# Optimization experiments

Hardware: AMD Instinct MI355X
Metric: run time of the kernel (lower is better)

## Reference

```python
import jax, jax.numpy as jnp
from jax import lax
import numpy as np

BN_EPS = 1e-5

def _bn(x, g, b, m, v):
    # inference-mode BatchNorm1d (running stats)
    return (x - m) * (g / jnp.sqrt(v + BN_EPS)) + b

def _mlp2(x, W1, g, b, m, v, W2):
    # Linear(no bias) -> BN -> ReLU -> (Dropout off in eval) -> Linear(no bias)
    h = jax.nn.relu(_bn(x @ W1.T, g, b, m, v))
    return h @ W2.T

def setup_inputs() -> dict:
    key = jax.random.key(0)
    ks = iter(jax.random.split(key, 40))
    B, N = 1024, 10
    f32 = jnp.float32
    def w(shape, s=0.02):
        return jax.random.normal(next(ks), shape, f32) * s
    def bn_params(c):
        return (jnp.ones((c,), f32), jnp.zeros((c,), f32),
                jax.random.normal(next(ks), (c,), f32) * 0.1,
                jax.random.uniform(next(ks), (c,), f32, 0.5, 1.5))
    inp = {
        'features_object': jax.random.normal(next(ks), (B, N, 1024), f32),
        'bbox': jax.random.uniform(next(ks), (B, N, 4), f32),
        'word_embedding': jax.random.normal(next(ks), (B, N, 300), f32),
        'sentiment': jax.random.normal(next(ks), (B, N, 4096), f32),
        'body': jax.random.normal(next(ks), (B, 2048), f32),
    }
    # mlp_object: 1024 -> 128 -> 128
    inp['W1_o'] = w((128, 1024)); inp['g_o'], inp['b_o'], inp['m_o'], inp['v_o'] = bn_params(128)
    inp['W2_o'] = w((128, 128))
    # mlp_sentiment: 4096 -> 512 -> 128
    inp['W1_s'] = w((512, 4096)); inp['g_s'], inp['b_s'], inp['m_s'], inp['v_s'] = bn_params(512)
    inp['W2_s'] = w((128, 512))
    # mlp_body: 2048 -> 256 -> 128
    inp['W1_b'] = w((256, 2048)); inp['g_b'], inp['b_b'], inp['m_b'], inp['v_b'] = bn_params(256)
    inp['W2_b'] = w((128, 256))
    # channel attention (CBAM-style, in_planes=10, ratio=2): shared MLP 10->5->10
    inp['Wc1'] = w((5, 10), 0.3)
    inp['Wc2'] = w((10, 5), 0.3)
    # spatial attention: Conv1d(2 -> 1, k=7, pad=3, no bias)
    inp['Wsa'] = w((1, 2, 7), 0.3)
    # fc1: 688 -> 256 (with bias) then BN
    inp['Wf'] = w((256, 688)); inp['bf'] = jnp.zeros((256,), f32)
    inp['g_f'], inp['b_f'], inp['m_f'], inp['v_f'] = bn_params(256)
    return inp

def reference(features_object, bbox, word_embedding, sentiment, body,
              W1_o, g_o, b_o, m_o, v_o, W2_o,
              W1_s, g_s, b_s, m_s, v_s, W2_s,
              W1_b, g_b, b_b, m_b, v_b, W2_b,
              Wc1, Wc2, Wsa, Wf, bf, g_f, b_f, m_f, v_f):
    B, N, _ = features_object.shape
    # per-slice MLPs batched into single GEMMs over B*N rows
    obj = _mlp2(features_object.reshape(B * N, -1), W1_o, g_o, b_o, m_o, v_o, W2_o).reshape(B, N, 128)
    sen = _mlp2(sentiment.reshape(B * N, -1), W1_s, g_s, b_s, m_s, v_s, W2_s).reshape(B, N, 128)
    # body is identical across the N repeats (inference BN), compute once and broadcast
    bod = _mlp2(body.reshape(B, -1), W1_b, g_b, b_b, m_b, v_b, W2_b)
    bod = jnp.broadcast_to(bod[:, None, :], (B, N, 128))
    x = jnp.concatenate([obj, bbox, word_embedding, sen, bod], axis=2)  # [B,N,688]
    # channel attention over the N-slice axis
    def ca_mlp(a):  # [B,N] -> [B,N]
        return jax.nn.relu(a @ Wc1.T) @ Wc2.T
    att_c = jax.nn.sigmoid(ca_mlp(x.mean(axis=2)) + ca_mlp(x.max(axis=2)))  # [B,N]
    x = x * att_c[:, :, None]
    # spatial attention along feature axis
    s = jnp.stack([x.mean(axis=1), x.max(axis=1)], axis=1)  # [B,2,688]
    sa = lax.conv_general_dilated(s, Wsa, (1,), [(3, 3)],
                                  dimension_numbers=('NCH', 'OIH', 'NCH'))  # [B,1,688]
    x = x * jax.nn.sigmoid(sa)
    x = x.sum(axis=1)  # [B,688]
    out = jax.nn.relu(_bn(x @ Wf.T + bf, g_f, b_f, m_f, v_f))  # [B,256]
    return out
```

## Files before the change

### kernel.cpp

```cpp
#include <hip/hip_runtime.h>
#include <hip/hip_bf16.h>
#include <math.h>

typedef __attribute__((ext_vector_type(8))) short short8;
typedef __attribute__((ext_vector_type(4))) float floatx4;

static __device__ __forceinline__ unsigned short f2bf(float f) {
    unsigned int u = __float_as_uint(f);
    unsigned int r = (u + 0x7fffu + ((u >> 16) & 1u)) >> 16;
    return (unsigned short)r;
}

static __device__ __forceinline__ void g2l16(const void* g, void* l) {
    __builtin_amdgcn_global_load_lds(
        (const __attribute__((address_space(1))) unsigned int*)g,
        (__attribute__((address_space(3))) unsigned int*)l,
        16, 0, 0);
}

struct GDesc {
    const float*          Af;
    const unsigned short* Ab;
    const unsigned short* W;
    float*          Cf;
    unsigned short* Cb;
    const float *bias, *g, *b, *m, *v;
    int M, N, K;
    int Kreal;
    int fuse;
    int nbx;
    int block0;
    int nbb;
    int ksplit;
};
struct GArgs { GDesc g[3]; int n; };

__global__ __launch_bounds__(256)
void gemm_grouped(GArgs ga)
{
    __shared__ unsigned short As[2][4096];
    __shared__ unsigned short Bs[2][4096];

    const int bid = blockIdx.x;
    int gi = 0;
    #pragma unroll
    for (int i = 1; i < 3; ++i)
        if (i < ga.n && bid >= ga.g[i].block0) gi = i;
    const GDesc d = ga.g[gi];

    int local = bid - d.block0;
    int kc = 0;
    int Kc = d.K;
    if (d.ksplit > 1) {
        Kc = d.K / d.ksplit;
        kc = local / d.nbb;
        local -= kc * d.nbb;
    }
    const int kbeg = kc * Kc;
    const int bx = local % d.nbx;
    const int by = local / d.nbx;
    const int row0 = by * 128;
    const int col0 = bx * 128;

    const int tid  = threadIdx.x;
    const int wave = tid >> 6;
    const int lane = tid & 63;
    const int qd   = lane >> 4;
    const int ln   = lane & 15;
    const int wr   = (wave >> 1) * 64;
    const int wc   = (wave & 1) * 64;

    const int c0 = wave * 128 + lane;
    const int c1 = c0 + 64;
    const int r0 = c0 >> 2, k0 = (c0 & 3) * 8;
    const int r1 = c1 >> 2, k1 = (c1 & 3) * 8;

    const int sr = tid >> 3;
    const int sc = (tid & 7) * 4;

    const bool afp = (d.Af != nullptr);
    const int niter = Kc >> 5;

    floatx4 acc[4][4];
    #pragma unroll
    for (int i = 0; i < 4; ++i)
        #pragma unroll
        for (int j = 0; j < 4; ++j) acc[i][j] = (floatx4){0.f, 0.f, 0.f, 0.f};

    g2l16(d.W + (size_t)(col0 + r0) * d.K + kbeg + k0, &Bs[0][(size_t)wave * 1024]);
    g2l16(d.W + (size_t)(col0 + r1) * d.K + kbeg + k1, &Bs[0][(size_t)wave * 1024 + 512]);
    float4 areg[4];
    if (afp) {
        #pragma unroll
        for (int p = 0; p < 4; ++p) {
            float4 v = (kbeg + sc < d.Kreal)
                ? *(const float4*)(d.Af + (size_t)(row0 + p * 32 + sr) * d.Kreal + kbeg + sc)
                : (float4){0.f, 0.f, 0.f, 0.f};
            ushort4 o = { f2bf(v.x), f2bf(v.y), f2bf(v.z), f2bf(v.w) };
            *(ushort4*)&As[0][(p * 32 + sr) * 32 + sc] = o;
        }
        if (niter > 1) {
            const int kg = kbeg + 32;
            #pragma unroll
            for (int p = 0; p < 4; ++p)
                areg[p] = (kg + sc < d.Kreal)
                    ? *(const float4*)(d.Af + (size_t)(row0 + p * 32 + sr) * d.Kreal + kg + sc)
                    : (float4){0.f, 0.f, 0.f, 0.f};
        }
    } else {
        g2l16(d.Ab + (size_t)(row0 + r0) * d.K + kbeg + k0, &As[0][(size_t)wave * 1024]);
        g2l16(d.Ab + (size_t)(row0 + r1) * d.K + kbeg + k1, &As[0][(size_t)wave * 1024 + 512]);
    }
    __syncthreads();

    int cur = 0;
    for (int it = 0; it < niter; ++it) {
        const int nxt = cur ^ 1;
        const bool pf = (it + 1 < niter);

        if (pf) {
            const int kg = kbeg + (it + 1) * 32;
            g2l16(d.W + (size_t)(col0 + r0) * d.K + kg + k0, &Bs[nxt][(size_t)wave * 1024]);
            g2l16(d.W + (size_t)(col0 + r1) * d.K + kg + k1, &Bs[nxt][(size_t)wave * 1024 + 512]);
            if (afp) {
                #pragma unroll
                for (int p = 0; p < 4; ++p) {
                    ushort4 o = { f2bf(areg[p].x), f2bf(areg[p].y),
                                  f2bf(areg[p].z), f2bf(areg[p].w) };
                    *(ushort4*)&As[nxt][(p * 32 + sr) * 32 + sc] = o;
                }
                if (it + 2 < niter) {
                    const int kg2 = kbeg + (it + 2) * 32;
                    #pragma unroll
                    for (int p = 0; p < 4; ++p)
                        areg[p] = (kg2 + sc < d.Kreal)
                            ? *(const float4*)(d.Af + (size_t)(row0 + p * 32 + sr) * d.Kreal + kg2 + sc)
                            : (float4){0.f, 0.f, 0.f, 0.f};
                }
            } else {
                g2l16(d.Ab + (size_t)(row0 + r0) * d.K + kg + k0, &As[nxt][(size_t)wave * 1024]);
                g2l16(d.Ab + (size_t)(row0 + r1) * d.K + kg + k1, &As[nxt][(size_t)wave * 1024 + 512]);
            }
        }

        short8 a[4], b[4];
        #pragma unroll
        for (int i = 0; i < 4; ++i)
            a[i] = *(const short8*)&As[cur][(wr + i * 16 + ln) * 32 + qd * 8];
        #pragma unroll
        for (int j = 0; j < 4; ++j)
            b[j] = *(const short8*)&Bs[cur][(wc + j * 16 + ln) * 32 + qd * 8];
        #pragma unroll
        for (int i = 0; i < 4; ++i)
            #pragma unroll
            for (int j = 0; j < 4; ++j)
                acc[i][j] = __builtin_amdgcn_mfma_f32_16x16x32_bf16(
                                a[i], b[j], acc[i][j], 0, 0, 0);

        __syncthreads();
        cur = nxt;
    }

    if (d.ksplit > 1) {
        #pragma unroll
        for (int j = 0; j < 4; ++j) {
            const int col = col0 + wc + j * 16 + ln;
            #pragma unroll
            for (int i = 0; i < 4; ++i) {
                #pragma unroll
                for (int r = 0; r < 4; ++r) {
                    const int row = row0 + wr + i * 16 + qd * 4 + r;
                    atomicAdd(&d.Cf[(size_t)row * d.N + col], acc[i][j][r]);
                }
            }
        }
        return;
    }

    #pragma unroll
    for (int j = 0; j < 4; ++j) {
        const int col = col0 + wc + j * 16 + ln;
        float add = d.bias ? d.bias[col] : 0.f;
        float scale = 1.f, shift = 0.f;
        if (d.fuse) {
            scale = d.g[col] * rsqrtf(d.v[col] + 1e-5f);
            shift = d.b[col] - d.m[col] * scale;
        }
        #pragma unroll
        for (int i = 0; i < 4; ++i) {
            #pragma unroll
            for (int r = 0; r < 4; ++r) {
                const int row = row0 + wr + i * 16 + qd * 4 + r;
                float vv = acc[i][j][r] + add;
                if (d.fuse) vv = fmaxf(vv * scale + shift, 0.f);
                if (d.Cf) d.Cf[(size_t)row * d.N + col] = vv;
                if (d.Cb) d.Cb[(size_t)row * d.N + col] = f2bf(vv);
            }
        }
    }
}

struct WSeg { const float* src; unsigned short* dst; int Kreal; int Kp; };
struct WArgs { WSeg s[7]; int off[8]; };

__global__ __launch_bounds__(256)
void cvt_weights(WArgs wa)
{
    int i = blockIdx.x * 256 + threadIdx.x;
    if (i >= wa.off[7]) return;
    int s = 0;
    #pragma unroll
    for (int j = 1; j < 7; ++j) if (i >= wa.off[j]) s = j;
    const WSeg sg = wa.s[s];
    const int li = i - wa.off[s];
    const int r = li / sg.Kp, c = li - r * sg.Kp;
    sg.dst[li] = (c < sg.Kreal) ? f2bf(sg.src[(size_t)r * sg.Kreal + c])
                                : (unsigned short)0;
}

struct FSeg { const float* src; unsigned short* dstb; float* dstf;
              const float *bias, *g, *b, *m, *v; int N; };
struct FArgs { FSeg s[3]; int off[4]; };

__global__ __launch_bounds__(256)
void bn_finalize(FArgs fa)
{
    int i = blockIdx.x * 256 + threadIdx.x;
    if (i >= fa.off[3]) return;
    int s = 0;
    #pragma unroll
    for (int j = 1; j < 3; ++j) if (i >= fa.off[j]) s = j;
    const FSeg sg = fa.s[s];
    const int li = i - fa.off[s];
    const int e = li * 4;
    const int col = e % sg.N;
    float4 vv = *(const float4*)(sg.src + e);
    float4 fo;
    ushort4 o;
    #pragma unroll
    for (int r = 0; r < 4; ++r) {
        float x = (&vv.x)[r];
        if (sg.bias) x += sg.bias[col + r];
        float sc = sg.g[col + r] * rsqrtf(sg.v[col + r] + 1e-5f);
        float sh = sg.b[col + r] - sg.m[col + r] * sc;
        x = fmaxf(x * sc + sh, 0.f);
        (&fo.x)[r] = x;
        ((unsigned short*)&o)[r] = f2bf(x);
    }
    if (sg.dstb) *(ushort4*)(sg.dstb + e) = o;
    if (sg.dstf) *(float4*)(sg.dstf + e) = fo;
}

__global__ __launch_bounds__(256)
void attn_kernel(const float* __restrict__ obj, const float* __restrict__ bbox,
                 const float* __restrict__ word, const float* __restrict__ sen,
                 const float* __restrict__ bod,
                 const float* __restrict__ Wc1, const float* __restrict__ Wc2,
                 const float* __restrict__ Wsa,
                 float* __restrict__ xsum_out)
{
    const int b = blockIdx.x;
    const int tid = threadIdx.x;

    __shared__ float xs[10][688];
    __shared__ float s0[688], s1[688];
    __shared__ float avec[10], mvec[10], att[10];
    __shared__ float cw[14], c1[50], c2[50];

    if (tid < 14) cw[tid] = Wsa[tid];
    if (tid < 50) { c1[tid] = Wc1[tid]; c2[tid] = Wc2[tid]; }

    for (int n = 0; n < 10; ++n) {
        const float* o  = obj  + ((size_t)b * 10 + n) * 128;
        const float* bx = bbox + ((size_t)b * 10 + n) * 4;
        const float* w  = word + ((size_t)b * 10 + n) * 300;
        const float* s  = sen  + ((size_t)b * 10 + n) * 128;
        const float* bo = bod  + (size_t)b * 128;
        for (int c = tid; c < 688; c += 256) {
            float v;
            if      (c < 128) v = o[c];
            else if (c < 132) v = bx[c - 128];
            else if (c < 432) v = w[c - 132];
            else if (c < 560) v = s[c - 432];
            else              v = bo[c - 560];
            xs[n][c] = v;
        }
    }
    __syncthreads();

    {
        const int wv = tid >> 6, ln2 = tid & 63;
        for (int n = wv; n < 10; n += 4) {
            float sm = 0.f, mx = -INFINITY;
            for (int c = ln2; c < 688; c += 64) {
                float v = xs[n][c];
                sm += v; mx = fmaxf(mx, v);
            }
            #pragma unroll
            for (int off = 32; off > 0; off >>= 1) {
                sm += __shfl_down(sm, off);
                mx = fmaxf(mx, __shfl_down(mx, off));
            }
            if (ln2 == 0) { avec[n] = sm * (1.f / 688.f); mvec[n] = mx; }
        }
    }
    __syncthreads();

    if (tid == 0) {
        float ha[5], hm[5];
        #pragma unroll
        for (int i = 0; i < 5; ++i) {
            float sa_ = 0.f, sm_ = 0.f;
            #pragma unroll
            for (int j = 0; j < 10; ++j) {
                sa_ += c1[i * 10 + j] * avec[j];
                sm_ += c1[i * 10 + j] * mvec[j];
            }
            ha[i] = fmaxf(sa_, 0.f);
            hm[i] = fmaxf(sm_, 0.f);
        }
        #pragma unroll
        for (int j = 0; j < 10; ++j) {
            float v = 0.f;
            #pragma unroll
            for (int i = 0; i < 5; ++i) v += c2[j * 5 + i] * (ha[i] + hm[i]);
            att[j] = 1.f / (1.f + expf(-v));
        }
    }
    __syncthreads();

    for (int c = tid; c < 688; c += 256) {
        float sm = 0.f, mx = -INFINITY;
        #pragma unroll
        for (int n = 0; n < 10; ++n) {
            float v = xs[n][c] * att[n];
            xs[n][c] = v;
            sm += v; mx = fmaxf(mx, v);
        }
        s0[c] = sm * 0.1f;
        s1[c] = mx;
    }
    __syncthreads();

    for (int c = tid; c < 688; c += 256) {
        float sa = 0.f;
        #pragma unroll
        for (int j = 0; j < 7; ++j) {
            int cc = c + j - 3;
            if (cc >= 0 && cc < 688)
                sa += cw[j] * s0[cc] + cw[7 + j] * s1[cc];
        }
        float sig = 1.f / (1.f + expf(-sa));
        float sm = 0.f;
        #pragma unroll
        for (int n = 0; n < 10; ++n) sm += xs[n][c];
        xsum_out[(size_t)b * 688 + c] = sm * sig;
    }
}

extern "C" void kernel_launch(void* const* d_in, const int* in_sizes, int n_in,
                              void* d_out, int out_size, void* d_ws, size_t ws_size,
                              hipStream_t stream)
{
    const float* f_obj = (const float*)d_in[0];
    const float* bbox  = (const float*)d_in[1];
    const float* word  = (const float*)d_in[2];
    const float* sent  = (const float*)d_in[3];
    const float* body  = (const float*)d_in[4];
    const float* W1_o  = (const float*)d_in[5];
    const float* g_o = (const float*)d_in[6],  *b_o = (const float*)d_in[7];
    const float* m_o = (const float*)d_in[8],  *v_o = (const float*)d_in[9];
    const float* W2_o  = (const float*)d_in[10];
    const float* W1_s  = (const float*)d_in[11];
    const float* g_s = (const float*)d_in[12], *b_s = (const float*)d_in[13];
    const float* m_s = (const float*)d_in[14], *v_s = (const float*)d_in[15];
    const float* W2_s  = (const float*)d_in[16];
    const float* W1_b  = (const float*)d_in[17];
    const float* g_b = (const float*)d_in[18], *b_b = (const float*)d_in[19];
    const float* m_b = (const float*)d_in[20], *v_b = (const float*)d_in[21];
    const float* W2_b  = (const float*)d_in[22];
    const float* Wc1 = (const float*)d_in[23];
    const float* Wc2 = (const float*)d_in[24];
    const float* Wsa = (const float*)d_in[25];
    const float* Wf  = (const float*)d_in[26];
    const float* bf  = (const float*)d_in[27];
    const float* g_f = (const float*)d_in[28], *b_f = (const float*)d_in[29];
    const float* m_f = (const float*)d_in[30], *v_f = (const float*)d_in[31];
    float* out = (float*)d_out;

    char* p = (char*)d_ws;
    unsigned short* w1s = (unsigned short*)p; p += 4194304;
    unsigned short* w2s = (unsigned short*)p; p += 131072;
    unsigned short* w1o = (unsigned short*)p; p += 262144;
    unsigned short* w2o = (unsigned short*)p; p += 32768;
    unsigned short* w1b = (unsigned short*)p; p += 1048576;
    unsigned short* w2b = (unsigned short*)p; p += 65536;
    unsigned short* wfp = (unsigned short*)p; p += 360448;
    unsigned short* h_s = (unsigned short*)p; p += 10485760;
    unsigned short* h_o = (unsigned short*)p; p += 2621440;
    unsigned short* h_b = (unsigned short*)p; p += 524288;
    char* region = p; p += 27262976;
    float* ps = (float*)region;
    float* po = (float*)(region + 20971520);
    float* pb = (float*)(region + 26214400);
    float* sen_f  = (float*)region;
    float* obj_f  = (float*)(region + 5242880);
    float* bod_f  = (float*)(region + 10485760);
    float* pf     = (float*)(region + 11010048);
    float* xsum_f = (float*)(region + 12058624);
    if ((size_t)(p - (char*)d_ws) > ws_size) return;

    hipMemsetAsync(region, 0, 27262976, stream);

    WArgs wa;
    wa.s[0] = { W1_s, w1s, 4096, 4096 };
    wa.s[1] = { W2_s, w2s,  512,  512 };
    wa.s[2] = { W1_o, w1o, 1024, 1024 };
    wa.s[3] = { W2_o, w2o,  128,  128 };
    wa.s[4] = { W1_b, w1b, 2048, 2048 };
    wa.s[5] = { W2_b, w2b,  256,  256 };
    wa.s[6] = { Wf,   wfp,  688,  704 };
    const int wn[7] = { 512*4096, 128*512, 128*1024, 128*128, 256*2048, 128*256, 256*704 };
    wa.off[0] = 0;
    for (int i = 0; i < 7; ++i) wa.off[i + 1] = wa.off[i] + wn[i];
    cvt_weights<<<(wa.off[7] + 255) / 256, 256, 0, stream>>>(wa);

    {
        GArgs ga; ga.n = 3;
        ga.g[0] = { sent,  nullptr, w1s, ps, nullptr, nullptr, nullptr, nullptr, nullptr, nullptr,
                    10240, 512, 4096, 4096, 0, 4, 0,    320, 4 };
        ga.g[1] = { f_obj, nullptr, w1o, po, nullptr, nullptr, nullptr, nullptr, nullptr, nullptr,
                    10240, 128, 1024, 1024, 0, 1, 1280, 80,  4 };
        ga.g[2] = { body,  nullptr, w1b, pb, nullptr, nullptr, nullptr, nullptr, nullptr, nullptr,
                    1024,  256, 2048, 2048, 0, 2, 1600, 16,  4 };
        gemm_grouped<<<1664, 256, 0, stream>>>(ga);
    }

    {
        FArgs fa;
        fa.s[0] = { ps, h_s, nullptr, nullptr, g_s, b_s, m_s, v_s, 512 };
        fa.s[1] = { po, h_o, nullptr, nullptr, g_o, b_o, m_o, v_o, 128 };
        fa.s[2] = { pb, h_b, nullptr, nullptr, g_b, b_b, m_b, v_b, 256 };
        fa.off[0] = 0;
        fa.off[1] = 10240 * 512 / 4;
        fa.off[2] = fa.off[1] + 10240 * 128 / 4;
        fa.off[3] = fa.off[2] + 1024 * 256 / 4;
        bn_finalize<<<(fa.off[3] + 255) / 256, 256, 0, stream>>>(fa);
    }

    hipMemsetAsync(region, 0, 12058624, stream);

    {
        GArgs ga; ga.n = 3;
        ga.g[0] = { nullptr, h_s, w2s, sen_f, nullptr, nullptr, nullptr, nullptr, nullptr, nullptr,
                    10240, 128, 512, 512, 0, 1, 0,   80, 4 };
        ga.g[1] = { nullptr, h_o, w2o, obj_f, nullptr, nullptr, nullptr, nullptr, nullptr, nullptr,
                    10240, 128, 128, 128, 0, 1, 320, 80, 2 };
        ga.g[2] = { nullptr, h_b, w2b, bod_f, nullptr, nullptr, nullptr, nullptr, nullptr, nullptr,
                    1024,  128, 256, 256, 0, 1, 480, 8,  2 };
        gemm_grouped<<<496, 256, 0, stream>>>(ga);
    }

    attn_kernel<<<1024, 256, 0, stream>>>(obj_f, bbox, word, sen_f, bod_f,
                                          Wc1, Wc2, Wsa, xsum_f);

    {
        GArgs ga; ga.n = 1;
        ga.g[0] = { xsum_f, nullptr, wfp, pf, nullptr, nullptr, nullptr, nullptr, nullptr, nullptr,
                    1024, 256, 704, 688, 0, 2, 0, 16, 11 };
        gemm_grouped<<<176, 256, 0, stream>>>(ga);
    }

    {
        FArgs fa;
        fa.s[0] = { pf, nullptr, out, bf, g_f, b_f, m_f, v_f, 256 };
        fa.s[1] = fa.s[0];
        fa.s[2] = fa.s[0];
        fa.off[0] = 0;
        fa.off[1] = 1024 * 256 / 4;
        fa.off[2] = fa.off[1];
        fa.off[3] = fa.off[1];
        bn_finalize<<<(fa.off[1] + 255) / 256, 256, 0, stream>>>(fa);
    }
}
```

Before: 578.8 us.

## Fold memsets into weight conversion, cut split-K, fuse final BN epilogue

Replaces the scalar bf16 rounding with the packed v_cvt_pk_bf16_f32 instruction when staging fp32 activations into LDS. Moves the workspace zeroing into the weight-conversion kernel and drops the second memset. Reduces the split-K factors of the first and second GEMM groups, with the second group going to no split. Runs the final fc GEMM without split-K and with its bias+BN+ReLU fused into the epilogue, which removes a separate finalize launch. Fewer blocks and fewer atomics trade parallelism for less partial-sum traffic and fewer launches.

```diff
diff --git a/kernel.cpp b/kernel.cpp
--- a/kernel.cpp
+++ b/kernel.cpp
@@ -9,6 +9,12 @@
     unsigned int u = __float_as_uint(f);
     unsigned int r = (u + 0x7fffu + ((u >> 16) & 1u)) >> 16;
     return (unsigned short)r;
+}
+
+static __device__ __forceinline__ unsigned int pk_bf16(float lo, float hi) {
+    unsigned int r;
+    asm("v_cvt_pk_bf16_f32 %0, %1, %2" : "=v"(r) : "v"(lo), "v"(hi));
+    return r;
 }
 
 static __device__ __forceinline__ void g2l16(const void* g, void* l) {
@@ -96,8 +102,8 @@
             float4 v = (kbeg + sc < d.Kreal)
                 ? *(const float4*)(d.Af + (size_t)(row0 + p * 32 + sr) * d.Kreal + kbeg + sc)
                 : (float4){0.f, 0.f, 0.f, 0.f};
-            ushort4 o = { f2bf(v.x), f2bf(v.y), f2bf(v.z), f2bf(v.w) };
-            *(ushort4*)&As[0][(p * 32 + sr) * 32 + sc] = o;
+            uint2 o = { pk_bf16(v.x, v.y), pk_bf16(v.z, v.w) };
+            *(uint2*)&As[0][(p * 32 + sr) * 32 + sc] = o;
         }
         if (niter > 1) {
             const int kg = kbeg + 32;
@@ -125,9 +131,9 @@
             if (afp) {
                 #pragma unroll
                 for (int p = 0; p < 4; ++p) {
-                    ushort4 o = { f2bf(areg[p].x), f2bf(areg[p].y),
-                                  f2bf(areg[p].z), f2bf(areg[p].w) };
-                    *(ushort4*)&As[nxt][(p * 32 + sr) * 32 + sc] = o;
+                    uint2 o = { pk_bf16(areg[p].x, areg[p].y),
+                                pk_bf16(areg[p].z, areg[p].w) };
+                    *(uint2*)&As[nxt][(p * 32 + sr) * 32 + sc] = o;
                 }
                 if (it + 2 < niter) {
                     const int kg2 = kbeg + (it + 2) * 32;
@@ -201,13 +207,17 @@
 }
 
 struct WSeg { const float* src; unsigned short* dst; int Kreal; int Kp; };
-struct WArgs { WSeg s[7]; int off[8]; };
+struct WArgs { WSeg s[7]; int off[8]; float4* zdst; int zn; };
 
 __global__ __launch_bounds__(256)
 void cvt_weights(WArgs wa)
 {
     int i = blockIdx.x * 256 + threadIdx.x;
-    if (i >= wa.off[7]) return;
+    if (i >= wa.off[7]) {
+        int z = i - wa.off[7];
+        if (z < wa.zn) wa.zdst[z] = (float4){0.f, 0.f, 0.f, 0.f};
+        return;
+    }
     int s = 0;
     #pragma unroll
     for (int j = 1; j < 7; ++j) if (i >= wa.off[j]) s = j;
@@ -406,11 +416,8 @@
     float* sen_f  = (float*)region;
     float* obj_f  = (float*)(region + 5242880);
     float* bod_f  = (float*)(region + 10485760);
-    float* pf     = (float*)(region + 11010048);
-    float* xsum_f = (float*)(region + 12058624);
+    float* xsum_f = (float*)(region + 11010048);
     if ((size_t)(p - (char*)d_ws) > ws_size) return;
-
-    hipMemsetAsync(region, 0, 27262976, stream);
 
     WArgs wa;
     wa.s[0] = { W1_s, w1s, 4096, 4096 };
@@ -423,17 +430,19 @@
     const int wn[7] = { 512*4096, 128*512, 128*1024, 128*128, 256*2048, 128*256, 256*704 };
     wa.off[0] = 0;
     for (int i = 0; i < 7; ++i) wa.off[i + 1] = wa.off[i] + wn[i];
-    cvt_weights<<<(wa.off[7] + 255) / 256, 256, 0, stream>>>(wa);
+    wa.zdst = (float4*)region;
+    wa.zn   = 27262976 / 16;
+    cvt_weights<<<(wa.off[7] + wa.zn + 255) / 256, 256, 0, stream>>>(wa);
 
     {
         GArgs ga; ga.n = 3;
         ga.g[0] = { sent,  nullptr, w1s, ps, nullptr, nullptr, nullptr, nullptr, nullptr, nullptr,
-                    10240, 512, 4096, 4096, 0, 4, 0,    320, 4 };
+                    10240, 512, 4096, 4096, 0, 4, 0,   320, 2 };
         ga.g[1] = { f_obj, nullptr, w1o, po, nullptr, nullptr, nullptr, nullptr, nullptr, nullptr,
-                    10240, 128, 1024, 1024, 0, 1, 1280, 80,  4 };
+                    10240, 128, 1024, 1024, 0, 1, 640, 80,  2 };
         ga.g[2] = { body,  nullptr, w1b, pb, nullptr, nullptr, nullptr, nullptr, nullptr, nullptr,
-                    1024,  256, 2048, 2048, 0, 2, 1600, 16,  4 };
-        gemm_grouped<<<1664, 256, 0, stream>>>(ga);
+                    1024,  256, 2048, 2048, 0, 2, 800, 16,  2 };
+        gemm_grouped<<<832, 256, 0, stream>>>(ga);
     }
 
     {
@@ -448,17 +457,15 @@
         bn_finalize<<<(fa.off[3] + 255) / 256, 256, 0, stream>>>(fa);
     }
 
-    hipMemsetAsync(region, 0, 12058624, stream);
-
     {
         GArgs ga; ga.n = 3;
         ga.g[0] = { nullptr, h_s, w2s, sen_f, nullptr, nullptr, nullptr, nullptr, nullptr, nullptr,
-                    10240, 128, 512, 512, 0, 1, 0,   80, 4 };
+                    10240, 128, 512, 512, 0, 1, 0,   80, 1 };
         ga.g[1] = { nullptr, h_o, w2o, obj_f, nullptr, nullptr, nullptr, nullptr, nullptr, nullptr,
-                    10240, 128, 128, 128, 0, 1, 320, 80, 2 };
+                    10240, 128, 128, 128, 0, 1, 80,  80, 1 };
         ga.g[2] = { nullptr, h_b, w2b, bod_f, nullptr, nullptr, nullptr, nullptr, nullptr, nullptr,
-                    1024,  128, 256, 256, 0, 1, 480, 8,  2 };
-        gemm_grouped<<<496, 256, 0, stream>>>(ga);
+                    1024,  128, 256, 256, 0, 1, 160, 8,  1 };
+        gemm_grouped<<<168, 256, 0, stream>>>(ga);
     }
 
     attn_kernel<<<1024, 256, 0, stream>>>(obj_f, bbox, word, sen_f, bod_f,
@@ -466,20 +473,8 @@
 
     {
         GArgs ga; ga.n = 1;
-        ga.g[0] = { xsum_f, nullptr, wfp, pf, nullptr, nullptr, nullptr, nullptr, nullptr, nullptr,
-                    1024, 256, 704, 688, 0, 2, 0, 16, 11 };
-        gemm_grouped<<<176, 256, 0, stream>>>(ga);
-    }
-
-    {
-        FArgs fa;
-        fa.s[0] = { pf, nullptr, out, bf, g_f, b_f, m_f, v_f, 256 };
-        fa.s[1] = fa.s[0];
-        fa.s[2] = fa.s[0];
-        fa.off[0] = 0;
-        fa.off[1] = 1024 * 256 / 4;
-        fa.off[2] = fa.off[1];
-        fa.off[3] = fa.off[1];
-        bn_finalize<<<(fa.off[1] + 255) / 256, 256, 0, stream>>>(fa);
-    }
-}
+        ga.g[0] = { xsum_f, nullptr, wfp, out, nullptr, bf, g_f, b_f, m_f, v_f,
+                    1024, 256, 704, 688, 1, 2, 0, 16, 1 };
+        gemm_grouped<<<16, 256, 0, stream>>>(ga);
+    }
+}
```

Result: faster. 537.6 us (-7.1%).
